# Optimization experiments

Hardware: AMD Instinct MI355X
Metric: run time of the kernel (lower is better)

Reference implementation:

```python
import jax, jax.numpy as jnp
import numpy as np

N_NODES = 50000
N_EDGES = 800000
NUM_GRAPHS = 256
NUM_SHAPES = 64
NODE_F = 128
EDGE_F = 16
H1 = 128   # embedding_size // 2
H2 = 256   # embedding_size
NEG_SLOPE_ATT = 0.2   # GATv2 attention LeakyReLU (PyG default)
NEG_SLOPE_ACT = 0.01  # torch.nn.LeakyReLU default
BN_EPS = 1e-5


def setup_inputs() -> dict:
    key = jax.random.key(0)
    ks = jax.random.split(key, 24)
    s = 0.05
    return {
        "x": jax.random.uniform(ks[0], (N_NODES, NUM_SHAPES), jnp.float32),
        "edge_index": jax.random.randint(ks[1], (2, N_EDGES), 0, N_NODES),
        "edge_attr": jax.random.normal(ks[2], (N_EDGES, EDGE_F), jnp.float32),
        "batch": jnp.sort(jax.random.randint(ks[3], (N_NODES,), 0, NUM_GRAPHS)),
        "emb_table": jax.random.normal(ks[4], (NUM_SHAPES, NODE_F), jnp.float32) * s,
        "Wl1": jax.random.normal(ks[5], (NODE_F, H1), jnp.float32) * s,
        "bl1": jnp.zeros((H1,), jnp.float32),
        "Wr1": jax.random.normal(ks[6], (NODE_F, H1), jnp.float32) * s,
        "br1": jnp.zeros((H1,), jnp.float32),
        "We1": jax.random.normal(ks[7], (EDGE_F, H1), jnp.float32) * s,
        "att1": jax.random.normal(ks[8], (H1,), jnp.float32) * s,
        "bias1": jnp.zeros((H1,), jnp.float32),
        "g1": jnp.ones((H1,), jnp.float32),
        "be1": jnp.zeros((H1,), jnp.float32),
        "Wl2": jax.random.normal(ks[9], (H1, H2), jnp.float32) * s,
        "bl2": jnp.zeros((H2,), jnp.float32),
        "Wr2": jax.random.normal(ks[10], (H1, H2), jnp.float32) * s,
        "br2": jnp.zeros((H2,), jnp.float32),
        "We2": jax.random.normal(ks[11], (EDGE_F, H2), jnp.float32) * s,
        "att2": jax.random.normal(ks[12], (H2,), jnp.float32) * s,
        "bias2": jnp.zeros((H2,), jnp.float32),
        "g2": jnp.ones((H2,), jnp.float32),
        "be2": jnp.zeros((H2,), jnp.float32),
        "Wg": jax.random.normal(ks[13], (H2, 1), jnp.float32) * s,
        "bg": jnp.zeros((1,), jnp.float32),
    }


def _add_self_loops(edge_index, edge_attr, n):
    # PyG GATv2Conv: add_self_loops=True, fill_value='mean' -> self-loop
    # edge_attr is the mean of incoming edge attrs (0 if node has no edges).
    src, dst = edge_index[0], edge_index[1]
    deg = jax.ops.segment_sum(jnp.ones_like(edge_attr[:, 0]), dst, num_segments=n)
    ea_mean = jax.ops.segment_sum(edge_attr, dst, num_segments=n) / jnp.maximum(deg, 1.0)[:, None]
    loop = jnp.arange(n)
    return (jnp.concatenate([src, loop]),
            jnp.concatenate([dst, loop]),
            jnp.concatenate([edge_attr, ea_mean], axis=0))


def _gatv2(x, src, dst, ea, Wl, bl, Wr, br, We, att, bias, n):
    xl = x @ Wl + bl                          # [N, C]
    xr = x @ Wr + br                          # [N, C]
    e = jax.nn.leaky_relu(xl[src] + xr[dst] + ea @ We, NEG_SLOPE_ATT)  # [E, C]
    logits = e @ att                          # [E]
    m = jax.ops.segment_max(logits, dst, num_segments=n)
    ex = jnp.exp(logits - m[dst])
    denom = jax.ops.segment_sum(ex, dst, num_segments=n)
    alpha = ex / denom[dst]                   # per-dst softmax (self-loops guarantee denom>0)
    out = jax.ops.segment_sum(xl[src] * alpha[:, None], dst, num_segments=n)
    return out + bias


def _batchnorm(x, g, b):
    mu = x.mean(0)
    var = ((x - mu) ** 2).mean(0)  # biased, as torch uses for normalization
    return (x - mu) * jax.lax.rsqrt(var + BN_EPS) * g + b


def reference(x, edge_index, edge_attr, batch, emb_table,
              Wl1, bl1, Wr1, br1, We1, att1, bias1, g1, be1,
              Wl2, bl2, Wr2, br2, We2, att2, bias2, g2, be2,
              Wg, bg):
    n = x.shape[0]
    h = emb_table[jnp.argmax(x, axis=1)]      # [N, NODE_F]
    src, dst, ea = _add_self_loops(edge_index, edge_attr, n)
    d1 = _gatv2(h, src, dst, ea, Wl1, bl1, Wr1, br1, We1, att1, bias1, n)
    d1 = jax.nn.leaky_relu(_batchnorm(d1, g1, be1), NEG_SLOPE_ACT)
    d2 = _gatv2(d1, src, dst, ea, Wl2, bl2, Wr2, br2, We2, att2, bias2, n)
    d2 = jax.nn.leaky_relu(_batchnorm(d2, g2, be2), NEG_SLOPE_ACT)
    # AttentionalAggregation: softmax(gate_nn(x)) over each graph, weighted sum
    gate = (d2 @ Wg + bg)[:, 0]               # [N]
    gm = jax.ops.segment_max(gate, batch, num_segments=NUM_GRAPHS)
    ge = jnp.exp(gate - gm[batch])
    gd = jax.ops.segment_sum(ge, batch, num_segments=NUM_GRAPHS)
    gd = jnp.where(gd == 0, 1.0, gd)
    w = ge / gd[batch]
    return jax.ops.segment_sum(d2 * w[:, None], batch, num_segments=NUM_GRAPHS)
```

## Files before the change

kernel.cpp:

```cpp
#include <hip/hip_runtime.h>
#include <cstddef>
#include <cstdint>

#define LEAKY_ATT 0.2f
#define LEAKY_ACT 0.01f
#define BN_EPS 1e-5f

typedef __attribute__((ext_vector_type(8))) short bf16x8;
typedef __attribute__((ext_vector_type(4))) float f32x4;
typedef __fp16 f16x2 __attribute__((ext_vector_type(2)));

static __device__ __forceinline__ unsigned short f2bf(float f){
  unsigned u = __float_as_uint(f);
  unsigned r = u + 0x7fffu + ((u >> 16) & 1u);
  return (unsigned short)(r >> 16);
}
static __device__ __forceinline__ float bf_lo(unsigned u){ return __uint_as_float(u << 16); }
static __device__ __forceinline__ float bf_hi(unsigned u){ return __uint_as_float(u & 0xffff0000u); }
static __device__ __forceinline__ float bf2f(unsigned short u){ return __uint_as_float((unsigned)u << 16); }

static __device__ __forceinline__ f16x2 cvtpk(float a, float b){
#if __has_builtin(__builtin_amdgcn_cvt_pkrtz)
  return __builtin_amdgcn_cvt_pkrtz(a, b);
#else
  f16x2 r; r.x = (__fp16)a; r.y = (__fp16)b; return r;
#endif
}
#if __has_builtin(__builtin_amdgcn_fdot2)
#define FDOT2(a,b,c) __builtin_amdgcn_fdot2((a),(b),(c),false)
#else
static __device__ __forceinline__ float fdot2_emu(f16x2 a, f16x2 b, float c){
  return (float)a.x*(float)b.x + ((float)a.y*(float)b.y + c);
}
#define FDOT2(a,b,c) fdot2_emu((a),(b),(c))
#endif

static __device__ __forceinline__ f16x2 bcast_pair(f16x2 v, int k){
  int iv; __builtin_memcpy(&iv, &v, 4);
  iv = __shfl(iv, k);
  f16x2 r; __builtin_memcpy(&r, &iv, 4);
  return r;
}

static __device__ __forceinline__ float wave_sum64(float x){
  float t;
  t = __int_as_float(__builtin_amdgcn_update_dpp(0, __float_as_int(x), 0x111, 0xf, 0xf, true)); x += t;
  t = __int_as_float(__builtin_amdgcn_update_dpp(0, __float_as_int(x), 0x112, 0xf, 0xf, true)); x += t;
  t = __int_as_float(__builtin_amdgcn_update_dpp(0, __float_as_int(x), 0x114, 0xf, 0xf, true)); x += t;
  t = __int_as_float(__builtin_amdgcn_update_dpp(0, __float_as_int(x), 0x118, 0xf, 0xf, true)); x += t;
  t = __int_as_float(__builtin_amdgcn_update_dpp(0, __float_as_int(x), 0x142, 0xf, 0xf, true)); x += t;
  t = __int_as_float(__builtin_amdgcn_update_dpp(0, __float_as_int(x), 0x143, 0xf, 0xf, true)); x += t;
  return __int_as_float(__builtin_amdgcn_readlane(__float_as_int(x), 63));
}

__global__ void k_embed(const float* __restrict__ x, const float* __restrict__ emb,
                        unsigned short* __restrict__ hb, int N){
  int wv = threadIdx.x >> 6, lane = threadIdx.x & 63;
  for (int n = blockIdx.x*4 + wv; n < N; n += gridDim.x*4){
    float v = x[(size_t)n*64 + lane];
    int idx = lane;
    #pragma unroll
    for (int off = 32; off; off >>= 1){
      float ov = __shfl_down(v, off);
      int   oi = __shfl_down(idx, off);
      if (ov > v || (ov == v && oi < idx)) { v = ov; idx = oi; }
    }
    idx = __shfl(idx, 0);
    hb[(size_t)n*128 + lane]      = f2bf(emb[(size_t)idx*128 + lane]);
    hb[(size_t)n*128 + 64 + lane] = f2bf(emb[(size_t)idx*128 + 64 + lane]);
  }
}

__global__ void k_deg(const int* __restrict__ dst, int* __restrict__ deg, int E){
  int e = blockIdx.x*blockDim.x + threadIdx.x;
  if (e >= E) return;
  atomicAdd(&deg[dst[e]], 1);
}

__global__ __launch_bounds__(256) void k_scan1(const int* __restrict__ deg,
                        int* __restrict__ rowptr, int* __restrict__ bsum, int N){
  __shared__ int sd[256];
  int tid = threadIdx.x;
  int base = blockIdx.x*1024 + tid*4;
  int v0=0,v1=0,v2=0,v3=0;
  if (base+0 < N) v0 = deg[base+0]+1;
  if (base+1 < N) v1 = deg[base+1]+1;
  if (base+2 < N) v2 = deg[base+2]+1;
  if (base+3 < N) v3 = deg[base+3]+1;
  int t = v0+v1+v2+v3;
  sd[tid] = t;
  __syncthreads();
  for (int off = 1; off < 256; off <<= 1){
    int x = (tid >= off) ? sd[tid-off] : 0;
    __syncthreads();
    sd[tid] += x;
    __syncthreads();
  }
  int excl = sd[tid] - t;
  if (tid == 255) bsum[blockIdx.x] = sd[255];
  if (base+0 < N) rowptr[base+0] = excl;
  if (base+1 < N) rowptr[base+1] = excl + v0;
  if (base+2 < N) rowptr[base+2] = excl + v0 + v1;
  if (base+3 < N) rowptr[base+3] = excl + v0 + v1 + v2;
}
__global__ void k_scan2(int* __restrict__ bsum, int nb){
  int lane = threadIdx.x & 63;
  int carry = 0;
  for (int base = 0; base < nb; base += 64){
    int idx = base + lane;
    int v = (idx < nb) ? bsum[idx] : 0;
    int orig = v;
    #pragma unroll
    for (int off = 1; off < 64; off <<= 1){
      int x = __shfl_up(v, off);
      if (lane >= off) v += x;
    }
    if (idx < nb) bsum[idx] = carry + v - orig;
    carry += __shfl(v, 63);
  }
}
__global__ void k_scan3(int* __restrict__ rowptr, const int* __restrict__ bsum,
                        int N, int EP){
  int i = blockIdx.x*blockDim.x + threadIdx.x;
  if (i < N) rowptr[i] += bsum[i >> 10];
  if (i == N) rowptr[N] = EP;
}

__global__ void k_csrfill(const int* __restrict__ src, const int* __restrict__ dst,
                          const int* __restrict__ rowptr,
                          int* __restrict__ cur, int2* __restrict__ csr2, int E, int N){
  int i = blockIdx.x*blockDim.x + threadIdx.x;
  if (i >= E + N) return;
  int d, s;
  if (i < E){ d = dst[i]; s = src[i]; }
  else      { d = i - E;  s = i - E;  }
  int pos = atomicAdd(&cur[d], 1);
  csr2[rowptr[d] + pos] = make_int2(s, i);
}

__global__ void k_wprep(const float* __restrict__ W, unsigned short* __restrict__ Wt,
                        int K, int C){
  int i = blockIdx.x*blockDim.x + threadIdx.x;
  if (i >= K*C) return;
  int n = i / K, k = i - n*K;
  Wt[i] = f2bf(W[(size_t)k*C + n]);
}

template<bool APPLY_BN>
__global__ __launch_bounds__(256) void k_gemm_mfma(
    const unsigned short* __restrict__ A,
    const unsigned short* __restrict__ Wtl, const float* __restrict__ bl,
    const unsigned short* __restrict__ Wtr, const float* __restrict__ br,
    const float* __restrict__ bnsc, const float* __restrict__ bnsh,
    unsigned short* __restrict__ xlb, float* __restrict__ xr,
    int N, int C)
{
  constexpr int K = 128;
  __shared__ unsigned short As[64][40];
  int tid = threadIdx.x;
  int wv = tid >> 6, lane = tid & 63;
  int m0 = blockIdx.x*64;
  int half = gridDim.y >> 1;
  bool isL = ((int)blockIdx.y < half);
  int n0 = (isL ? blockIdx.y : blockIdx.y - half) * 128;
  const unsigned short* Wt = isL ? Wtl : Wtr;
  const float* bias = isL ? bl : br;

  f32x4 acc[8];
  #pragma unroll
  for (int t = 0; t < 8; ++t) acc[t] = (f32x4){0.f,0.f,0.f,0.f};

  int srow = tid >> 2;
  int sseg = (tid & 3) * 8;
  int grow = m0 + srow;
  int arow = wv*16 + (lane & 15);
  int koff = (lane >> 4) * 8;

  for (int k0 = 0; k0 < K; k0 += 32){
    __syncthreads();
    uint4 raw = make_uint4(0,0,0,0);
    if (grow < N){
      raw = *reinterpret_cast<const uint4*>(&A[(size_t)grow*K + k0 + sseg]);
      if constexpr (APPLY_BN){
        float4 sa = *reinterpret_cast<const float4*>(&bnsc[k0 + sseg]);
        float4 sb = *reinterpret_cast<const float4*>(&bnsc[k0 + sseg + 4]);
        float4 ha = *reinterpret_cast<const float4*>(&bnsh[k0 + sseg]);
        float4 hb = *reinterpret_cast<const float4*>(&bnsh[k0 + sseg + 4]);
        float f0 = bf_lo(raw.x)*sa.x + ha.x; f0 = (f0>=0.f)?f0:LEAKY_ACT*f0;
        float f1 = bf_hi(raw.x)*sa.y + ha.y; f1 = (f1>=0.f)?f1:LEAKY_ACT*f1;
        float f2 = bf_lo(raw.y)*sa.z + ha.z; f2 = (f2>=0.f)?f2:LEAKY_ACT*f2;
        float f3 = bf_hi(raw.y)*sa.w + ha.w; f3 = (f3>=0.f)?f3:LEAKY_ACT*f3;
        float f4 = bf_lo(raw.z)*sb.x + hb.x; f4 = (f4>=0.f)?f4:LEAKY_ACT*f4;
        float f5 = bf_hi(raw.z)*sb.y + hb.y; f5 = (f5>=0.f)?f5:LEAKY_ACT*f5;
        float f6 = bf_lo(raw.w)*sb.z + hb.z; f6 = (f6>=0.f)?f6:LEAKY_ACT*f6;
        float f7 = bf_hi(raw.w)*sb.w + hb.w; f7 = (f7>=0.f)?f7:LEAKY_ACT*f7;
        raw.x = (unsigned)f2bf(f0) | ((unsigned)f2bf(f1) << 16);
        raw.y = (unsigned)f2bf(f2) | ((unsigned)f2bf(f3) << 16);
        raw.z = (unsigned)f2bf(f4) | ((unsigned)f2bf(f5) << 16);
        raw.w = (unsigned)f2bf(f6) | ((unsigned)f2bf(f7) << 16);
      }
    }
    *reinterpret_cast<uint4*>(&As[srow][sseg]) = raw;
    __syncthreads();
    bf16x8 a = *reinterpret_cast<const bf16x8*>(&As[arow][koff]);
    #pragma unroll
    for (int nt = 0; nt < 8; ++nt){
      int ncol = n0 + nt*16 + (lane & 15);
      bf16x8 b = *reinterpret_cast<const bf16x8*>(&Wt[(size_t)ncol*K + k0 + koff]);
      acc[nt] = __builtin_amdgcn_mfma_f32_16x16x32_bf16(a, b, acc[nt], 0, 0, 0);
    }
  }
  int rbase = m0 + wv*16 + (lane >> 4)*4;
  #pragma unroll
  for (int nt = 0; nt < 8; ++nt){
    int col = n0 + nt*16 + (lane & 15);
    float bv = bias[col];
    #pragma unroll
    for (int r = 0; r < 4; ++r){
      int row = rbase + r;
      if (row < N){
        float v = acc[nt][r] + bv;
        if (isL) xlb[(size_t)row*C + col] = f2bf(v);
        else     xr [(size_t)row*C + col] = v;
      }
    }
  }
}

template<int C, int UNR, bool OUTBF>
__global__ __launch_bounds__(64) void k_gat_fused(
    const int* __restrict__ rowptr, const int2* __restrict__ csr2,
    const float* __restrict__ edge_attr,
    const unsigned short* __restrict__ xlb, const float* __restrict__ xr,
    const float* __restrict__ We, const float* __restrict__ att,
    const float* __restrict__ bias, float* __restrict__ out_f,
    unsigned short* __restrict__ out_b, int E, int N)
{
  constexpr int CPL = C/64;
  constexpr int PK  = CPL/2;
  const int lane = threadIdx.x;
  const int c0 = lane*CPL;

  f16x2 wpk[8][CPL];
  #pragma unroll
  for (int k8 = 0; k8 < 8; ++k8)
    #pragma unroll
    for (int q = 0; q < CPL; ++q)
      wpk[k8][q] = cvtpk(We[(2*k8)*C + c0 + q], We[(2*k8+1)*C + c0 + q]);
  float attv[CPL], biasv[CPL];
  #pragma unroll
  for (int q = 0; q < CPL; ++q){ attv[q] = att[c0 + q]; biasv[q] = bias[c0 + q]; }

  for (int n = blockIdx.x; n < N; n += gridDim.x){
    float xrv[CPL];
    #pragma unroll
    for (int q = 0; q < CPL; ++q) xrv[q] = xr[(size_t)n*C + c0 + q];
    int start = __builtin_amdgcn_readfirstlane(rowptr[n]);
    int end   = __builtin_amdgcn_readfirstlane(rowptr[n+1]);

    float denom = 0.f;
    float acc[CPL] = {};
    float2 easum = make_float2(0.f, 0.f);

    unsigned xA[UNR][PK]; f16x2 eaA[UNR];
    unsigned xB[UNR][PK]; f16x2 eaB[UNR];

    auto stage = [&](int base, unsigned (&xp)[UNR][PK], f16x2 (&eal)[UNR])->int{
      int mask = 0;
      #pragma unroll
      for (int u = 0; u < UNR; ++u){
        bool zero = true;
        if (base + u < end){
          int2 v = csr2[base + u];
          int e = __builtin_amdgcn_readfirstlane(v.y);
          if (e < E){
            int s = __builtin_amdgcn_readfirstlane(v.x);
            float2 ep = *reinterpret_cast<const float2*>(
                &edge_attr[(size_t)e*16 + 2*(lane & 7)]);
            easum.x += ep.x; easum.y += ep.y;
            eal[u] = cvtpk(ep.x, ep.y);
            const unsigned short* prow = xlb + (size_t)s*C + c0;
            if constexpr (PK == 2){
              uint2 w = *reinterpret_cast<const uint2*>(prow);
              xp[u][0] = w.x; xp[u][1] = w.y;
            } else {
              xp[u][0] = *reinterpret_cast<const unsigned*>(prow);
            }
            mask |= 1 << u;
            zero = false;
          }
        }
        if (zero){
          eal[u] = cvtpk(0.f, 0.f);
          #pragma unroll
          for (int p = 0; p < PK; ++p) xp[u][p] = 0;
        }
      }
      return mask;
    };
    auto compute = [&](unsigned (&xp)[UNR][PK], f16x2 (&eal)[UNR], int mask){
      float pe[UNR];
      #pragma unroll
      for (int u = 0; u < UNR; ++u){
        if ((mask >> u) & 1){
          float w[CPL] = {};
          #pragma unroll
          for (int k8 = 0; k8 < 8; ++k8){
            f16x2 pr = bcast_pair(eal[u], k8);
            #pragma unroll
            for (int q = 0; q < CPL; ++q) w[q] = FDOT2(pr, wpk[k8][q], w[q]);
          }
          float p = 0.f;
          #pragma unroll
          for (int p2 = 0; p2 < PK; ++p2){
            float x0 = bf_lo(xp[u][p2]), x1 = bf_hi(xp[u][p2]);
            float v0 = x0 + xrv[2*p2]   + w[2*p2];
            float v1 = x1 + xrv[2*p2+1] + w[2*p2+1];
            v0 = (v0 >= 0.f) ? v0 : LEAKY_ATT*v0;
            v1 = (v1 >= 0.f) ? v1 : LEAKY_ATT*v1;
            p += attv[2*p2]*v0 + attv[2*p2+1]*v1;
          }
          p = wave_sum64(p);
          pe[u] = __expf(p);
        } else pe[u] = 0.f;
      }
      #pragma unroll
      for (int u = 0; u < UNR; ++u) denom += pe[u];
      #pragma unroll
      for (int u = 0; u < UNR; ++u)
        #pragma unroll
        for (int p2 = 0; p2 < PK; ++p2){
          acc[2*p2]   += pe[u]*bf_lo(xp[u][p2]);
          acc[2*p2+1] += pe[u]*bf_hi(xp[u][p2]);
        }
    };

    int i = start;
    int mA = stage(i, xA, eaA);
    int mB = 0;
    for (;;){
      int j = i + UNR;
      if (j < end) mB = stage(j, xB, eaB);
      compute(xA, eaA, mA);
      i = j;
      if (i >= end) break;
      j = i + UNR;
      if (j < end) mA = stage(j, xA, eaA);
      compute(xB, eaB, mB);
      i = j;
      if (i >= end) break;
    }

    {
      int deg = end - start - 1;
      float invd = 1.0f / (float)max(deg, 1);
      eaA[0] = cvtpk(easum.x*invd, easum.y*invd);
      const unsigned short* prow = xlb + (size_t)n*C + c0;
      if constexpr (PK == 2){
        uint2 w = *reinterpret_cast<const uint2*>(prow);
        xA[0][0] = w.x; xA[0][1] = w.y;
      } else {
        xA[0][0] = *reinterpret_cast<const unsigned*>(prow);
      }
      compute(xA, eaA, 1);
    }

    float inv = 1.0f / denom;
    if constexpr (OUTBF){
      #pragma unroll
      for (int p2 = 0; p2 < PK; ++p2){
        unsigned po = (unsigned)f2bf(acc[2*p2]*inv + biasv[2*p2])
                    | ((unsigned)f2bf(acc[2*p2+1]*inv + biasv[2*p2+1]) << 16);
        *reinterpret_cast<unsigned*>(&out_b[(size_t)n*C + c0 + 2*p2]) = po;
      }
    } else {
      if constexpr (CPL == 4){
        float4 o = make_float4(acc[0]*inv + biasv[0], acc[1]*inv + biasv[1],
                               acc[2]*inv + biasv[2], acc[3]*inv + biasv[3]);
        *reinterpret_cast<float4*>(&out_f[(size_t)n*C + c0]) = o;
      } else {
        float2 o = make_float2(acc[0]*inv + biasv[0], acc[1]*inv + biasv[1]);
        *reinterpret_cast<float2*>(&out_f[(size_t)n*C + c0]) = o;
      }
    }
  }
}

__global__ void k_bnstats(const float* __restrict__ x, float* __restrict__ sums,
                          int N, int C){
  int c = threadIdx.x;
  float s = 0.f, s2 = 0.f;
  for (int r = blockIdx.x; r < N; r += gridDim.x){
    float v = x[(size_t)r*C + c];
    s += v; s2 += v*v;
  }
  atomicAdd(&sums[c], s);
  atomicAdd(&sums[C + c], s2);
}

__global__ void k_bnstats_bf(const unsigned short* __restrict__ x,
                             float* __restrict__ sums, int N, int C){
  int c = threadIdx.x;
  float s = 0.f, s2 = 0.f;
  for (int r = blockIdx.x; r < N; r += gridDim.x){
    float v = bf2f(x[(size_t)r*C + c]);
    s += v; s2 += v*v;
  }
  atomicAdd(&sums[c], s);
  atomicAdd(&sums[C + c], s2);
}

__global__ void k_bnfin(const float* __restrict__ sums, const float* __restrict__ gam,
                        const float* __restrict__ bet, float* __restrict__ sc,
                        float* __restrict__ sh, int N, int C){
  int c = threadIdx.x; if (c >= C) return;
  float invN = 1.0f / (float)N;
  float mu  = sums[c] * invN;
  float var = sums[C + c] * invN - mu*mu;
  float r = rsqrtf(var + BN_EPS) * gam[c];
  sc[c] = r;
  sh[c] = bet[c] - mu*r;
}

__global__ __launch_bounds__(256) void k_bngate_final(
    const float* __restrict__ d2, const float* __restrict__ sc2,
    const float* __restrict__ sh2, const float* __restrict__ Wg,
    const float* __restrict__ bg, const int* __restrict__ gptr,
    float* __restrict__ out)
{
  int g = blockIdx.x;
  int s = gptr[g], e = gptr[g+1];
  int tid = threadIdx.x, wv = tid >> 6, lane = tid & 63;
  __shared__ float red[4];
  float scv = sc2[tid], shv = sh2[tid], wgv = Wg[tid], bgv = bg[0];
  float den = 0.f, acc = 0.f;
  float xv = (s < e) ? d2[(size_t)s*256 + tid] : 0.f;
  for (int n = s; n < e; ++n){
    float xn = (n+1 < e) ? d2[(size_t)(n+1)*256 + tid] : 0.f;
    float v = xv*scv + shv;
    v = (v >= 0.f) ? v : LEAKY_ACT*v;
    float p = wave_sum64(v * wgv);
    if (lane == 0) red[wv] = p;
    __syncthreads();
    float gt = (red[0] + red[1]) + (red[2] + red[3]) + bgv;
    __syncthreads();
    float ex = __expf(gt);
    den += ex;
    acc += ex * v;
    xv = xn;
  }
  out[(size_t)g*256 + tid] = (e > s) ? acc/den : 0.f;
}

__global__ void k_gptr(const int* __restrict__ batch, int* __restrict__ gptr, int N, int G){
  int n = blockIdx.x*blockDim.x + threadIdx.x;
  if (n > N) return;
  if (n == N){
    int last = batch[N-1];
    for (int g = last+1; g <= G; ++g) gptr[g] = N;
    return;
  }
  int bc = batch[n];
  int bp = (n == 0) ? -1 : batch[n-1];
  for (int g = bp+1; g <= bc; ++g) gptr[g] = n;
}

extern "C" void kernel_launch(void* const* d_in, const int* in_sizes, int n_in,
                              void* d_out, int out_size, void* d_ws, size_t ws_size,
                              hipStream_t stream){
  const float* x         = (const float*)d_in[0];
  const int*   edge_idx  = (const int*)  d_in[1];
  const float* edge_attr = (const float*)d_in[2];
  const int*   batch     = (const int*)  d_in[3];
  const float* emb       = (const float*)d_in[4];
  const float* Wl1 = (const float*)d_in[5];  const float* bl1 = (const float*)d_in[6];
  const float* Wr1 = (const float*)d_in[7];  const float* br1 = (const float*)d_in[8];
  const float* We1 = (const float*)d_in[9];  const float* att1= (const float*)d_in[10];
  const float* bias1=(const float*)d_in[11]; const float* g1  = (const float*)d_in[12];
  const float* be1 = (const float*)d_in[13];
  const float* Wl2 = (const float*)d_in[14]; const float* bl2 = (const float*)d_in[15];
  const float* Wr2 = (const float*)d_in[16]; const float* br2 = (const float*)d_in[17];
  const float* We2 = (const float*)d_in[18]; const float* att2= (const float*)d_in[19];
  const float* bias2=(const float*)d_in[20]; const float* g2  = (const float*)d_in[21];
  const float* be2 = (const float*)d_in[22];
  const float* Wg  = (const float*)d_in[23]; const float* bg  = (const float*)d_in[24];
  float* out = (float*)d_out;

  const int N = in_sizes[0] / 64;
  const int E = in_sizes[1] / 2;
  const int EP = E + N;
  const int G = 256;
  const int* srcv = edge_idx;
  const int* dstv = edge_idx + E;

  float* ws = (float*)d_ws;
  size_t o = 0;
  auto alloc = [&](size_t elems){ size_t r = o; o += (elems + 63) & ~(size_t)63; return r; };
  size_t o_big1  = alloc((size_t)N*128);
  size_t o_union = alloc((size_t)N*256);
  size_t o_xlb1  = alloc((size_t)N*64);
  size_t o_xr2   = alloc((size_t)N*256);
  size_t o_bn1   = alloc(2*128);
  size_t o_bn2   = alloc(2*256);
  size_t o_sc1   = alloc(128);
  size_t o_sh1   = alloc(128);
  size_t o_sc2   = alloc(256);
  size_t o_sh2   = alloc(256);
  size_t o_deg   = alloc((size_t)N);
  size_t o_cur   = alloc((size_t)N);
  size_t o_rp    = alloc((size_t)N+1);
  size_t o_bsum  = alloc(64);
  size_t o_csr   = alloc((size_t)EP*2);
  size_t o_wt1l  = alloc(128*128/2);
  size_t o_wt1r  = alloc(128*128/2);
  size_t o_wt2l  = alloc(256*128/2);
  size_t o_wt2r  = alloc(256*128/2);
  size_t o_gptr  = alloc(G+1);

  unsigned short* hb   = (unsigned short*)(ws + o_big1);
  unsigned short* xlb2 = (unsigned short*)(ws + o_big1);
  float* xr1  = ws + o_union;
  unsigned short* d1b = (unsigned short*)(ws + o_union + (size_t)N*128);
  float* d2   = ws + o_union;
  unsigned short* xlb1 = (unsigned short*)(ws + o_xlb1);
  float* xr2  = ws + o_xr2;
  float* bn1  = ws + o_bn1;
  float* bn2  = ws + o_bn2;
  float* sc1  = ws + o_sc1;
  float* sh1  = ws + o_sh1;
  float* sc2  = ws + o_sc2;
  float* sh2  = ws + o_sh2;
  int*   deg  = (int*)(ws + o_deg);
  int*   cur  = (int*)(ws + o_cur);
  int*   rp   = (int*)(ws + o_rp);
  int*   bsum = (int*)(ws + o_bsum);
  int2*  csr2 = (int2*)(ws + o_csr);
  unsigned short* wt1l = (unsigned short*)(ws + o_wt1l);
  unsigned short* wt1r = (unsigned short*)(ws + o_wt1r);
  unsigned short* wt2l = (unsigned short*)(ws + o_wt2l);
  unsigned short* wt2r = (unsigned short*)(ws + o_wt2r);
  int*   gptr = (int*)(ws + o_gptr);

  hipMemsetAsync(deg, 0, (o_cur - o_deg + (size_t)N)*4, stream);
  hipMemsetAsync(bn1, 0, (o_bn2 - o_bn1 + 2*256)*4, stream);

  auto nblk = [](long long n, int b){ return (int)((n + b - 1) / b); };

  k_embed<<<1024, 256, 0, stream>>>(x, emb, hb, N);
  k_deg<<<nblk(E,256), 256, 0, stream>>>(dstv, deg, E);
  int nbs = nblk(N, 1024);
  k_scan1<<<nbs, 256, 0, stream>>>(deg, rp, bsum, N);
  k_scan2<<<1, 64, 0, stream>>>(bsum, nbs);
  k_scan3<<<nblk((long long)N+1,256), 256, 0, stream>>>(rp, bsum, N, EP);
  k_csrfill<<<nblk(EP,256), 256, 0, stream>>>(srcv, dstv, rp, cur, csr2, E, N);
  k_wprep<<<nblk(128*128,256), 256, 0, stream>>>(Wl1, wt1l, 128, 128);
  k_wprep<<<nblk(128*128,256), 256, 0, stream>>>(Wr1, wt1r, 128, 128);
  k_wprep<<<nblk(128*256,256), 256, 0, stream>>>(Wl2, wt2l, 128, 256);
  k_wprep<<<nblk(128*256,256), 256, 0, stream>>>(Wr2, wt2r, 128, 256);

  const int FGRID = 8192;

  {
    dim3 grid(nblk(N,64), 2);
    k_gemm_mfma<false><<<grid, 256, 0, stream>>>(hb, wt1l, bl1, wt1r, br1,
        nullptr, nullptr, xlb1, xr1, N, 128);
  }
  k_gat_fused<128,8,true><<<FGRID, 64, 0, stream>>>(rp, csr2, edge_attr,
      xlb1, xr1, We1, att1, bias1, nullptr, d1b, E, N);
  k_bnstats_bf<<<512, 128, 0, stream>>>(d1b, bn1, N, 128);
  k_bnfin<<<1, 128, 0, stream>>>(bn1, g1, be1, sc1, sh1, N, 128);

  {
    dim3 grid(nblk(N,64), 4);
    k_gemm_mfma<true><<<grid, 256, 0, stream>>>(d1b, wt2l, bl2, wt2r, br2,
        sc1, sh1, xlb2, xr2, N, 256);
  }
  k_gat_fused<256,6,false><<<FGRID, 64, 0, stream>>>(rp, csr2, edge_attr,
      xlb2, xr2, We2, att2, bias2, d2, nullptr, E, N);
  k_bnstats<<<512, 256, 0, stream>>>(d2, bn2, N, 256);
  k_bnfin<<<1, 256, 0, stream>>>(bn2, g2, be2, sc2, sh2, N, 256);

  k_gptr<<<nblk((long long)N+1,256), 256, 0, stream>>>(batch, gptr, N, G);
  k_bngate_final<<<G, 256, 0, stream>>>(d2, sc2, sh2, Wg, bg, gptr, out);
}
```

Measured before the change: 843.7 us.

## Fuse batchnorm statistics into GAT kernel and parallelize final gate pooling

Per-channel sum and sum-of-squares for batchnorm are accumulated in registers inside the fused GAT kernel and flushed with atomics, removing the separate stats kernels that reread node features. The final gated pooling kernel now processes nodes in parallel across 16 waves with float4 loads instead of a serial per-node loop with block barriers. Grid size and the layer-2 unroll factor are also increased. This adds per-block atomics and more register pressure in the GAT kernel.

```diff
diff --git a/kernel.cpp b/kernel.cpp
--- a/kernel.cpp
+++ b/kernel.cpp
@@ -234,7 +234,8 @@
     const unsigned short* __restrict__ xlb, const float* __restrict__ xr,
     const float* __restrict__ We, const float* __restrict__ att,
     const float* __restrict__ bias, float* __restrict__ out_f,
-    unsigned short* __restrict__ out_b, int E, int N)
+    unsigned short* __restrict__ out_b, float* __restrict__ bnsums,
+    int E, int N)
 {
   constexpr int CPL = C/64;
   constexpr int PK  = CPL/2;
@@ -250,6 +251,8 @@
   float attv[CPL], biasv[CPL];
   #pragma unroll
   for (int q = 0; q < CPL; ++q){ attv[q] = att[c0 + q]; biasv[q] = bias[c0 + q]; }
+
+  float bnS[CPL] = {}, bnS2[CPL] = {};
 
   for (int n = blockIdx.x; n < N; n += gridDim.x){
     float xrv[CPL];
@@ -366,48 +369,36 @@
     }
 
     float inv = 1.0f / denom;
+    float ov[CPL];
+    #pragma unroll
+    for (int q = 0; q < CPL; ++q){
+      ov[q] = acc[q]*inv + biasv[q];
+      bnS[q]  += ov[q];
+      bnS2[q] += ov[q]*ov[q];
+    }
     if constexpr (OUTBF){
       #pragma unroll
       for (int p2 = 0; p2 < PK; ++p2){
-        unsigned po = (unsigned)f2bf(acc[2*p2]*inv + biasv[2*p2])
-                    | ((unsigned)f2bf(acc[2*p2+1]*inv + biasv[2*p2+1]) << 16);
+        unsigned po = (unsigned)f2bf(ov[2*p2])
+                    | ((unsigned)f2bf(ov[2*p2+1]) << 16);
         *reinterpret_cast<unsigned*>(&out_b[(size_t)n*C + c0 + 2*p2]) = po;
       }
     } else {
       if constexpr (CPL == 4){
-        float4 o = make_float4(acc[0]*inv + biasv[0], acc[1]*inv + biasv[1],
-                               acc[2]*inv + biasv[2], acc[3]*inv + biasv[3]);
+        float4 o = make_float4(ov[0], ov[1], ov[2], ov[3]);
         *reinterpret_cast<float4*>(&out_f[(size_t)n*C + c0]) = o;
       } else {
-        float2 o = make_float2(acc[0]*inv + biasv[0], acc[1]*inv + biasv[1]);
+        float2 o = make_float2(ov[0], ov[1]);
         *reinterpret_cast<float2*>(&out_f[(size_t)n*C + c0]) = o;
       }
     }
   }
-}
-
-__global__ void k_bnstats(const float* __restrict__ x, float* __restrict__ sums,
-                          int N, int C){
-  int c = threadIdx.x;
-  float s = 0.f, s2 = 0.f;
-  for (int r = blockIdx.x; r < N; r += gridDim.x){
-    float v = x[(size_t)r*C + c];
-    s += v; s2 += v*v;
-  }
-  atomicAdd(&sums[c], s);
-  atomicAdd(&sums[C + c], s2);
-}
-
-__global__ void k_bnstats_bf(const unsigned short* __restrict__ x,
-                             float* __restrict__ sums, int N, int C){
-  int c = threadIdx.x;
-  float s = 0.f, s2 = 0.f;
-  for (int r = blockIdx.x; r < N; r += gridDim.x){
-    float v = bf2f(x[(size_t)r*C + c]);
-    s += v; s2 += v*v;
-  }
-  atomicAdd(&sums[c], s);
-  atomicAdd(&sums[C + c], s2);
+
+  #pragma unroll
+  for (int q = 0; q < CPL; ++q){
+    atomicAdd(&bnsums[c0 + q],     bnS[q]);
+    atomicAdd(&bnsums[C + c0 + q], bnS2[q]);
+  }
 }
 
 __global__ void k_bnfin(const float* __restrict__ sums, const float* __restrict__ gam,
@@ -422,34 +413,45 @@
   sh[c] = bet[c] - mu*r;
 }
 
-__global__ __launch_bounds__(256) void k_bngate_final(
+__global__ __launch_bounds__(1024) void k_bngate_final(
     const float* __restrict__ d2, const float* __restrict__ sc2,
     const float* __restrict__ sh2, const float* __restrict__ Wg,
     const float* __restrict__ bg, const int* __restrict__ gptr,
     float* __restrict__ out)
 {
+  __shared__ float lacc[16][256];
+  __shared__ float lden[16];
   int g = blockIdx.x;
   int s = gptr[g], e = gptr[g+1];
   int tid = threadIdx.x, wv = tid >> 6, lane = tid & 63;
-  __shared__ float red[4];
-  float scv = sc2[tid], shv = sh2[tid], wgv = Wg[tid], bgv = bg[0];
-  float den = 0.f, acc = 0.f;
-  float xv = (s < e) ? d2[(size_t)s*256 + tid] : 0.f;
-  for (int n = s; n < e; ++n){
-    float xn = (n+1 < e) ? d2[(size_t)(n+1)*256 + tid] : 0.f;
-    float v = xv*scv + shv;
-    v = (v >= 0.f) ? v : LEAKY_ACT*v;
-    float p = wave_sum64(v * wgv);
-    if (lane == 0) red[wv] = p;
-    __syncthreads();
-    float gt = (red[0] + red[1]) + (red[2] + red[3]) + bgv;
-    __syncthreads();
-    float ex = __expf(gt);
+  int c0 = lane*4;
+  float4 scv = *reinterpret_cast<const float4*>(&sc2[c0]);
+  float4 shv = *reinterpret_cast<const float4*>(&sh2[c0]);
+  float4 wgv = *reinterpret_cast<const float4*>(&Wg[c0]);
+  float bgv = bg[0];
+  float den = 0.f;
+  float a0 = 0.f, a1 = 0.f, a2 = 0.f, a3 = 0.f;
+  for (int n = s + wv; n < e; n += 16){
+    float4 xv = *reinterpret_cast<const float4*>(&d2[(size_t)n*256 + c0]);
+    float v0 = xv.x*scv.x + shv.x;  v0 = (v0 >= 0.f) ? v0 : LEAKY_ACT*v0;
+    float v1 = xv.y*scv.y + shv.y;  v1 = (v1 >= 0.f) ? v1 : LEAKY_ACT*v1;
+    float v2 = xv.z*scv.z + shv.z;  v2 = (v2 >= 0.f) ? v2 : LEAKY_ACT*v2;
+    float v3 = xv.w*scv.w + shv.w;  v3 = (v3 >= 0.f) ? v3 : LEAKY_ACT*v3;
+    float p = wave_sum64(v0*wgv.x + v1*wgv.y + v2*wgv.z + v3*wgv.w) + bgv;
+    float ex = __expf(p);
     den += ex;
-    acc += ex * v;
-    xv = xn;
-  }
-  out[(size_t)g*256 + tid] = (e > s) ? acc/den : 0.f;
+    a0 += ex*v0; a1 += ex*v1; a2 += ex*v2; a3 += ex*v3;
+  }
+  lacc[wv][c0+0] = a0; lacc[wv][c0+1] = a1;
+  lacc[wv][c0+2] = a2; lacc[wv][c0+3] = a3;
+  if (lane == 0) lden[wv] = den;
+  __syncthreads();
+  if (tid < 256){
+    float at = 0.f, dt = 0.f;
+    #pragma unroll
+    for (int w = 0; w < 16; ++w){ at += lacc[w][tid]; dt += lden[w]; }
+    out[(size_t)g*256 + tid] = (e > s) ? at/dt : 0.f;
+  }
 }
 
 __global__ void k_gptr(const int* __restrict__ batch, int* __restrict__ gptr, int N, int G){
@@ -558,7 +560,7 @@
   k_wprep<<<nblk(128*256,256), 256, 0, stream>>>(Wl2, wt2l, 128, 256);
   k_wprep<<<nblk(128*256,256), 256, 0, stream>>>(Wr2, wt2r, 128, 256);
 
-  const int FGRID = 8192;
+  const int FGRID = 16384;
 
   {
     dim3 grid(nblk(N,64), 2);
@@ -566,8 +568,7 @@
         nullptr, nullptr, xlb1, xr1, N, 128);
   }
   k_gat_fused<128,8,true><<<FGRID, 64, 0, stream>>>(rp, csr2, edge_attr,
-      xlb1, xr1, We1, att1, bias1, nullptr, d1b, E, N);
-  k_bnstats_bf<<<512, 128, 0, stream>>>(d1b, bn1, N, 128);
+      xlb1, xr1, We1, att1, bias1, nullptr, d1b, bn1, E, N);
   k_bnfin<<<1, 128, 0, stream>>>(bn1, g1, be1, sc1, sh1, N, 128);
 
   {
@@ -575,11 +576,10 @@
     k_gemm_mfma<true><<<grid, 256, 0, stream>>>(d1b, wt2l, bl2, wt2r, br2,
         sc1, sh1, xlb2, xr2, N, 256);
   }
-  k_gat_fused<256,6,false><<<FGRID, 64, 0, stream>>>(rp, csr2, edge_attr,
-      xlb2, xr2, We2, att2, bias2, d2, nullptr, E, N);
-  k_bnstats<<<512, 256, 0, stream>>>(d2, bn2, N, 256);
+  k_gat_fused<256,8,false><<<FGRID, 64, 0, stream>>>(rp, csr2, edge_attr,
+      xlb2, xr2, We2, att2, bias2, d2, nullptr, bn2, E, N);
   k_bnfin<<<1, 256, 0, stream>>>(bn2, g2, be2, sc2, sh2, N, 256);
 
   k_gptr<<<nblk((long long)N+1,256), 256, 0, stream>>>(batch, gptr, N, G);
-  k_bngate_final<<<G, 256, 0, stream>>>(d2, sc2, sh2, Wg, bg, gptr, out);
-}
+  k_bngate_final<<<G, 1024, 0, stream>>>(d2, sc2, sh2, Wg, bg, gptr, out);
+}
```

Result: slower. 2.704 ms (+220.5%).

## Parallelize attentional pooling across waves with vectorized per-node processing

Applied to the files above, without the earlier changes.

The gate/pooling kernel now uses 1024 threads per graph. Each of 16 waves processes a different node, and each lane handles four channels with float4 loads. This removes the per-node block-wide synchronizations and the serial node loop. Partial numerators and denominators are combined in shared memory at the end, at the cost of extra LDS usage and a final reduction.

```diff
diff --git a/kernel.cpp b/kernel.cpp
--- a/kernel.cpp
+++ b/kernel.cpp
@@ -422,34 +422,45 @@
   sh[c] = bet[c] - mu*r;
 }
 
-__global__ __launch_bounds__(256) void k_bngate_final(
+__global__ __launch_bounds__(1024) void k_bngate_final(
     const float* __restrict__ d2, const float* __restrict__ sc2,
     const float* __restrict__ sh2, const float* __restrict__ Wg,
     const float* __restrict__ bg, const int* __restrict__ gptr,
     float* __restrict__ out)
 {
+  __shared__ float lacc[16][256];
+  __shared__ float lden[16];
   int g = blockIdx.x;
   int s = gptr[g], e = gptr[g+1];
   int tid = threadIdx.x, wv = tid >> 6, lane = tid & 63;
-  __shared__ float red[4];
-  float scv = sc2[tid], shv = sh2[tid], wgv = Wg[tid], bgv = bg[0];
-  float den = 0.f, acc = 0.f;
-  float xv = (s < e) ? d2[(size_t)s*256 + tid] : 0.f;
-  for (int n = s; n < e; ++n){
-    float xn = (n+1 < e) ? d2[(size_t)(n+1)*256 + tid] : 0.f;
-    float v = xv*scv + shv;
-    v = (v >= 0.f) ? v : LEAKY_ACT*v;
-    float p = wave_sum64(v * wgv);
-    if (lane == 0) red[wv] = p;
-    __syncthreads();
-    float gt = (red[0] + red[1]) + (red[2] + red[3]) + bgv;
-    __syncthreads();
-    float ex = __expf(gt);
+  int c0 = lane*4;
+  float4 scv = *reinterpret_cast<const float4*>(&sc2[c0]);
+  float4 shv = *reinterpret_cast<const float4*>(&sh2[c0]);
+  float4 wgv = *reinterpret_cast<const float4*>(&Wg[c0]);
+  float bgv = bg[0];
+  float den = 0.f;
+  float a0 = 0.f, a1 = 0.f, a2 = 0.f, a3 = 0.f;
+  for (int n = s + wv; n < e; n += 16){
+    float4 xv = *reinterpret_cast<const float4*>(&d2[(size_t)n*256 + c0]);
+    float v0 = xv.x*scv.x + shv.x;  v0 = (v0 >= 0.f) ? v0 : LEAKY_ACT*v0;
+    float v1 = xv.y*scv.y + shv.y;  v1 = (v1 >= 0.f) ? v1 : LEAKY_ACT*v1;
+    float v2 = xv.z*scv.z + shv.z;  v2 = (v2 >= 0.f) ? v2 : LEAKY_ACT*v2;
+    float v3 = xv.w*scv.w + shv.w;  v3 = (v3 >= 0.f) ? v3 : LEAKY_ACT*v3;
+    float p = wave_sum64(v0*wgv.x + v1*wgv.y + v2*wgv.z + v3*wgv.w) + bgv;
+    float ex = __expf(p);
     den += ex;
-    acc += ex * v;
-    xv = xn;
-  }
-  out[(size_t)g*256 + tid] = (e > s) ? acc/den : 0.f;
+    a0 += ex*v0; a1 += ex*v1; a2 += ex*v2; a3 += ex*v3;
+  }
+  lacc[wv][c0+0] = a0; lacc[wv][c0+1] = a1;
+  lacc[wv][c0+2] = a2; lacc[wv][c0+3] = a3;
+  if (lane == 0) lden[wv] = den;
+  __syncthreads();
+  if (tid < 256){
+    float at = 0.f, dt = 0.f;
+    #pragma unroll
+    for (int w = 0; w < 16; ++w){ at += lacc[w][tid]; dt += lden[w]; }
+    out[(size_t)g*256 + tid] = (e > s) ? at/dt : 0.f;
+  }
 }
 
 __global__ void k_gptr(const int* __restrict__ batch, int* __restrict__ gptr, int N, int G){
@@ -581,5 +592,5 @@
   k_bnfin<<<1, 256, 0, stream>>>(bn2, g2, be2, sc2, sh2, N, 256);
 
   k_gptr<<<nblk((long long)N+1,256), 256, 0, stream>>>(batch, gptr, N, G);
-  k_bngate_final<<<G, 256, 0, stream>>>(d2, sc2, sh2, Wg, bg, gptr, out);
-}
+  k_bngate_final<<<G, 1024, 0, stream>>>(d2, sc2, sh2, Wg, bg, gptr, out);
+}
```

After: 747.0 us. 11.5% less time.
